# Performance work log

Measured on AMD Instinct MI355X. Metric: run time of the kernel, lower is better.

Reference implementation:

```python
import jax, jax.numpy as jnp
import numpy as np

G, NP, K, H, DH, D, NL = 256, 1000, 8, 8, 10, 80, 10  # graphs, nodes/graph, knn, heads, d_head, hidden, layers


def setup_inputs() -> dict:
    key = jax.random.key(0)
    ks = jax.random.split(key, 16)
    rn = lambda k, shape: (jax.random.normal(k, shape, jnp.float32) * 0.05)
    return dict(
        h_feat=jax.random.normal(ks[0], (G, NP, 9), jnp.float32),
        bn_gamma=jnp.ones((9,), jnp.float32), bn_beta=jnp.zeros((9,), jnp.float32),
        W_emb=rn(ks[1], (9, D)), b_emb=jnp.zeros((D,), jnp.float32),
        Wq=rn(ks[2], (NL, D, D)), Wk=rn(ks[3], (NL, D, D)), Wv=rn(ks[4], (NL, D, D)),
        Wo=rn(ks[5], (NL, D, D)), bo=jnp.zeros((NL, D), jnp.float32),
        W1=rn(ks[6], (NL, D, 2 * D)), b1=jnp.zeros((NL, 2 * D), jnp.float32),
        W2=rn(ks[7], (NL, 2 * D, D)), b2=jnp.zeros((NL, D), jnp.float32),
        Wr0=rn(ks[8], (D, 40)), br0=jnp.zeros((40,), jnp.float32),
        Wr1=rn(ks[9], (40, 20)), br1=jnp.zeros((20,), jnp.float32),
        Wr2=rn(ks[10], (20, 64)), br2=jnp.zeros((64,), jnp.float32),
        W_clust=rn(ks[11], (64, 3)),
        W_beta=rn(ks[12], (64, 1)), b_beta=jnp.zeros((1,), jnp.float32),
    )


def _forward(h_feat, bn_gamma, bn_beta, W_emb, b_emb, Wq, Wk, Wv, Wo, bo,
             W1, b1, W2, b2, Wr0, br0, Wr1, br1, Wr2, br2, W_clust, W_beta, b_beta):
    # knn graph on raw coords (first 3 feature columns), per graph, k=8 (self included)
    coords = h_feat[..., :3]
    d2 = jnp.sum((coords[:, :, None, :] - coords[:, None, :, :]) ** 2, -1)  # [G,NP,NP]
    nbr = jax.lax.top_k(-d2, K)[1]  # [G,NP,K] neighbor indices per destination node
    gidx = jnp.arange(G)[:, None, None]

    # BatchNorm1d (training-mode batch stats over all nodes) + embedding
    x = h_feat.reshape(-1, 9)
    mu = x.mean(0)
    var = x.var(0)
    x = (x - mu) / jnp.sqrt(var + 1e-5) * bn_gamma + bn_beta
    h = (x @ W_emb + b_emb).reshape(G, NP, D)

    inv_sqrt_d = jnp.float32(1.0 / np.sqrt(DH))

    def layer(h, p):
        wq, wk, wv, wo, bo_, w1, b1_, w2, b2_ = p
        q = (h @ wq).reshape(G, NP, H, DH)
        k_ = (h @ wk).reshape(G, NP, H, DH)
        v = (h @ wv).reshape(G, NP, H, DH)
        kn = k_[gidx, nbr]  # [G,NP,K,H,DH] gather src K over edges
        vn = v[gidx, nbr]
        s = jnp.einsum('gnkhd,gnhd->gnkh', kn, q) * inv_sqrt_d
        s = jnp.exp(jnp.clip(s, -5.0, 5.0))  # scaled_exp with clamp
        wV = jnp.einsum('gnkh,gnkhd->gnhd', s, vn)
        attn = (wV / (s.sum(2)[..., None] + 1e-6)).reshape(G, NP, D)
        h = h + attn @ wo + bo_  # O proj + residual (no LN/BN)
        h = h + jax.nn.relu(h @ w1 + b1_) @ w2 + b2_  # FFN + residual
        return h, None

    h, _ = jax.lax.scan(layer, h, (Wq, Wk, Wv, Wo, bo, W1, b1, W2, b2))

    # MLPReadout 80->40->20->64 (ReLU between), then clustering coords + beta
    y = h.reshape(-1, D)
    y = jax.nn.relu(y @ Wr0 + br0)
    y = jax.nn.relu(y @ Wr1 + br1)
    y = y @ Wr2 + br2
    cc = y @ W_clust  # [N,3], no bias
    beta = y @ W_beta + b_beta  # [N,1]
    return jnp.concatenate([cc, beta], axis=1)  # [N,4]


def reference(h_feat, bn_gamma, bn_beta, W_emb, b_emb, Wq, Wk, Wv, Wo, bo,
              W1, b1, W2, b2, Wr0, br0, Wr1, br1, Wr2, br2, W_clust, W_beta, b_beta):
    return _forward(h_feat, bn_gamma, bn_beta, W_emb, b_emb, Wq, Wk, Wv, Wo, bo,
                    W1, b1, W2, b2, Wr0, br0, Wr1, br1, Wr2, br2, W_clust, W_beta, b_beta)
```

## Files before the change

kernel.cpp:

```cpp
#include <hip/hip_runtime.h>
#include <cstdint>
#include <cstddef>


typedef __attribute__((ext_vector_type(8))) short short8v;
typedef __attribute__((ext_vector_type(4))) float f32x4;

#define MFMA16(ACC, A, B) ACC = __builtin_amdgcn_mfma_f32_16x16x32_bf16(A, B, ACC, 0, 0, 0)
#define MF3(ACC, AH, AL, BH, BL) { MFMA16(ACC, AH, BH); MFMA16(ACC, AH, BL); MFMA16(ACC, AL, BH); }

__device__ __forceinline__ void splitbf(float x, unsigned short& hi, unsigned short& lo) {
  unsigned u = __float_as_uint(x);
  unsigned r = u + 0x7FFFu + ((u >> 16) & 1u);
  hi = (unsigned short)(r >> 16);
  float hf = __uint_as_float(((unsigned)hi) << 16);
  float lf = x - hf;
  unsigned u2 = __float_as_uint(lf);
  unsigned r2 = u2 + 0x7FFFu + ((u2 >> 16) & 1u);
  lo = (unsigned short)(r2 >> 16);
}

__device__ __forceinline__ float bf2f(unsigned short v) {
  return __uint_as_float(((unsigned)v) << 16);
}

__global__ __launch_bounds__(256) void knn_kernel(const float* __restrict__ hf, int* __restrict__ nbr) {
  __shared__ __align__(16) float cs[3000];
  int b = blockIdx.x;
  int g = b >> 2;
  for (int i = threadIdx.x; i < 3000; i += 256) {
    cs[i] = hf[((size_t)g * 1000 + (i / 3)) * 9 + (i % 3)];
  }
  __syncthreads();
  int tid = threadIdx.x;
  int lane = tid & 127;
  int q = ((b & 3) << 1) + (tid >> 7);
  if (lane < 125) {
    int n = q * 125 + lane;
    float cx = cs[n * 3 + 0], cy = cs[n * 3 + 1], cz = cs[n * 3 + 2];
    float bd[8];
    int bi[8];
    #pragma unroll
    for (int q2 = 0; q2 < 8; ++q2) { bd[q2] = 3.402823466e38f; bi[q2] = 0; }
    for (int j = 0; j < 1000; j += 8) {
      const float4* base = reinterpret_cast<const float4*>(cs + j * 3);
      float4 a0 = base[0], a1 = base[1], a2 = base[2], a3 = base[3], a4 = base[4], a5 = base[5];
      float d2v[8];
      {
        float dx = __fsub_rn(cx, a0.x), dy = __fsub_rn(cy, a0.y), dz = __fsub_rn(cz, a0.z);
        d2v[0] = __fadd_rn(__fadd_rn(__fmul_rn(dx, dx), __fmul_rn(dy, dy)), __fmul_rn(dz, dz));
      }
      {
        float dx = __fsub_rn(cx, a0.w), dy = __fsub_rn(cy, a1.x), dz = __fsub_rn(cz, a1.y);
        d2v[1] = __fadd_rn(__fadd_rn(__fmul_rn(dx, dx), __fmul_rn(dy, dy)), __fmul_rn(dz, dz));
      }
      {
        float dx = __fsub_rn(cx, a1.z), dy = __fsub_rn(cy, a1.w), dz = __fsub_rn(cz, a2.x);
        d2v[2] = __fadd_rn(__fadd_rn(__fmul_rn(dx, dx), __fmul_rn(dy, dy)), __fmul_rn(dz, dz));
      }
      {
        float dx = __fsub_rn(cx, a2.y), dy = __fsub_rn(cy, a2.z), dz = __fsub_rn(cz, a2.w);
        d2v[3] = __fadd_rn(__fadd_rn(__fmul_rn(dx, dx), __fmul_rn(dy, dy)), __fmul_rn(dz, dz));
      }
      {
        float dx = __fsub_rn(cx, a3.x), dy = __fsub_rn(cy, a3.y), dz = __fsub_rn(cz, a3.z);
        d2v[4] = __fadd_rn(__fadd_rn(__fmul_rn(dx, dx), __fmul_rn(dy, dy)), __fmul_rn(dz, dz));
      }
      {
        float dx = __fsub_rn(cx, a3.w), dy = __fsub_rn(cy, a4.x), dz = __fsub_rn(cz, a4.y);
        d2v[5] = __fadd_rn(__fadd_rn(__fmul_rn(dx, dx), __fmul_rn(dy, dy)), __fmul_rn(dz, dz));
      }
      {
        float dx = __fsub_rn(cx, a4.z), dy = __fsub_rn(cy, a4.w), dz = __fsub_rn(cz, a5.x);
        d2v[6] = __fadd_rn(__fadd_rn(__fmul_rn(dx, dx), __fmul_rn(dy, dy)), __fmul_rn(dz, dz));
      }
      {
        float dx = __fsub_rn(cx, a5.y), dy = __fsub_rn(cy, a5.z), dz = __fsub_rn(cz, a5.w);
        d2v[7] = __fadd_rn(__fadd_rn(__fmul_rn(dx, dx), __fmul_rn(dy, dy)), __fmul_rn(dz, dz));
      }
      #pragma unroll
      for (int u = 0; u < 8; ++u) {
        float d2 = d2v[u];
        if (d2 < bd[7]) {
          bd[7] = d2; bi[7] = j + u;
          #pragma unroll
          for (int q2 = 7; q2 >= 1; --q2) {
            if (bd[q2] < bd[q2 - 1]) {
              float tf = bd[q2]; bd[q2] = bd[q2 - 1]; bd[q2 - 1] = tf;
              int ti = bi[q2]; bi[q2] = bi[q2 - 1]; bi[q2 - 1] = ti;
            }
          }
        }
      }
    }
    #pragma unroll
    for (int kk = 0; kk < 8; ++kk) nbr[((size_t)g * 1000 + n) * 8 + kk] = bi[kk];
  }
}

__global__ __launch_bounds__(256) void bn_stat1(const float* __restrict__ hf, float* __restrict__ partial) {
  __shared__ float red[4][18];
  int row = blockIdx.x * 256 + threadIdx.x;
  float s[9], ss[9];
  #pragma unroll
  for (int f = 0; f < 9; ++f) {
    float v = hf[(size_t)row * 9 + f];
    s[f] = v;
    ss[f] = v * v;
  }
  for (int off = 32; off > 0; off >>= 1) {
    #pragma unroll
    for (int f = 0; f < 9; ++f) {
      s[f] += __shfl_down(s[f], off);
      ss[f] += __shfl_down(ss[f], off);
    }
  }
  int wid = threadIdx.x >> 6, lane = threadIdx.x & 63;
  if (lane == 0) {
    #pragma unroll
    for (int f = 0; f < 9; ++f) { red[wid][f] = s[f]; red[wid][9 + f] = ss[f]; }
  }
  __syncthreads();
  if (threadIdx.x < 18) {
    partial[(size_t)blockIdx.x * 18 + threadIdx.x] =
        red[0][threadIdx.x] + red[1][threadIdx.x] + red[2][threadIdx.x] + red[3][threadIdx.x];
  }
}

__global__ __launch_bounds__(256) void bn_stat2(const float* __restrict__ partial, float* __restrict__ stats) {
  __shared__ double sd[9][28], qd[9][28];
  int tid = threadIdx.x;
  if (tid < 252) {
    int f = tid % 9, gq = tid / 9;
    double s = 0.0, q = 0.0;
    for (int b = gq; b < 1000; b += 28) {
      s += (double)partial[b * 18 + f];
      q += (double)partial[b * 18 + 9 + f];
    }
    sd[f][gq] = s;
    qd[f][gq] = q;
  }
  __syncthreads();
  if (tid < 9) {
    double s = 0.0, q = 0.0;
    for (int g2 = 0; g2 < 28; ++g2) { s += sd[tid][g2]; q += qd[tid][g2]; }
    double mu = s / 256000.0;
    double var = q / 256000.0 - mu * mu;
    stats[tid] = (float)mu;
    stats[9 + tid] = (float)(1.0 / sqrt(var + 1e-5));
  }
}

__global__ __launch_bounds__(256) void split_tr(const float* __restrict__ src, unsigned short* __restrict__ dhi,
                                                unsigned short* __restrict__ dlo, int R, int C, int KS) {
  const float* s = src + (size_t)blockIdx.x * R * C;
  unsigned short* dh = dhi + (size_t)blockIdx.x * C * KS;
  unsigned short* dl = dlo + (size_t)blockIdx.x * C * KS;
  int n = C * KS;
  for (int i = threadIdx.x; i < n; i += 256) {
    int c = i / KS, kk = i % KS;
    float v = (kk < R) ? s[kk * C + c] : 0.f;
    unsigned short h, l;
    splitbf(v, h, l);
    dh[i] = h;
    dl[i] = l;
  }
}

__global__ __launch_bounds__(320) void embed_kernel(const float* __restrict__ hf, const float* __restrict__ stats,
                                                    const float* __restrict__ gamma, const float* __restrict__ beta,
                                                    const float* __restrict__ We, const float* __restrict__ be,
                                                    float* __restrict__ h) {
  __shared__ __align__(16) float xs[40 * 9];
  size_t p0 = (size_t)blockIdx.x * 40;
  for (int i = threadIdx.x; i < 360; i += 320) {
    int f = i % 9;
    float x = hf[p0 * 9 + i];
    xs[i] = (x - stats[f]) * stats[9 + f] * gamma[f] + beta[f];
  }
  __syncthreads();
  int c = threadIdx.x % 80, pg = threadIdx.x / 80;
  float we[9];
  #pragma unroll
  for (int f = 0; f < 9; ++f) we[f] = We[f * 80 + c];
  float bias = be[c];
  for (int pp = 0; pp < 10; ++pp) {
    int p = pg * 10 + pp;
    float acc = 0.f;
    #pragma unroll
    for (int f = 0; f < 9; ++f) acc = fmaf(xs[p * 9 + f], we[f], acc);
    h[(p0 + p) * 80 + c] = acc + bias;
  }
}

__global__ __launch_bounds__(320) void kv_kernel(const float* __restrict__ h,
                                                 const unsigned short* __restrict__ WkH, const unsigned short* __restrict__ WkL,
                                                 const unsigned short* __restrict__ WvH, const unsigned short* __restrict__ WvL,
                                                 float* __restrict__ kb, float* __restrict__ vb) {
  __shared__ __align__(16) unsigned short ahi[48 * 104];
  __shared__ __align__(16) unsigned short alo[48 * 104];
  int b = blockIdx.x;
  int xcd = b & 7;
  int r = b >> 3;
  int graph = (xcd << 5) + (r / 25);
  int jb = r % 25;
  size_t p0 = (size_t)graph * 1000 + (size_t)jb * 40;
  int tid = threadIdx.x;
  int lane = tid & 63, wv = tid >> 6;
  int fr = lane & 15, fq = lane >> 4;
  for (int i = tid; i < 800; i += 320) {
    int row = i / 20, kq = i % 20;
    float4 v = reinterpret_cast<const float4*>(h + (p0 + row) * 80)[kq];
    unsigned short h0, l0, h1, l1, h2, l2, h3, l3;
    splitbf(v.x, h0, l0); splitbf(v.y, h1, l1); splitbf(v.z, h2, l2); splitbf(v.w, h3, l3);
    int off = row * 104 + kq * 4;
    *reinterpret_cast<unsigned*>(&ahi[off]) = (unsigned)h0 | ((unsigned)h1 << 16);
    *reinterpret_cast<unsigned*>(&ahi[off + 2]) = (unsigned)h2 | ((unsigned)h3 << 16);
    *reinterpret_cast<unsigned*>(&alo[off]) = (unsigned)l0 | ((unsigned)l1 << 16);
    *reinterpret_cast<unsigned*>(&alo[off + 2]) = (unsigned)l2 | ((unsigned)l3 << 16);
  }
  for (int i = tid; i < 384; i += 320) {
    int row = i >> 3, kk = 80 + ((i & 7) << 1);
    int off = row * 104 + kk;
    *reinterpret_cast<unsigned*>(&ahi[off]) = 0u;
    *reinterpret_cast<unsigned*>(&alo[off]) = 0u;
  }
  __syncthreads();
  int bcol = wv * 16 + fr;
  f32x4 ck0 = {0.f, 0.f, 0.f, 0.f}, ck1 = ck0, ck2 = ck0;
  f32x4 cv0 = ck0, cv1 = ck0, cv2 = ck0;
  #pragma unroll
  for (int ks = 0; ks < 3; ++ks) {
    int boff = bcol * 96 + ks * 32 + fq * 8;
    short8v bkh = *reinterpret_cast<const short8v*>(WkH + boff);
    short8v bkl = *reinterpret_cast<const short8v*>(WkL + boff);
    short8v bvh = *reinterpret_cast<const short8v*>(WvH + boff);
    short8v bvl = *reinterpret_cast<const short8v*>(WvL + boff);
    int a0 = (0 * 16 + fr) * 104 + ks * 32 + fq * 8;
    int a1 = (1 * 16 + fr) * 104 + ks * 32 + fq * 8;
    int a2 = (2 * 16 + fr) * 104 + ks * 32 + fq * 8;
    short8v ah0 = *reinterpret_cast<const short8v*>(ahi + a0);
    short8v al0 = *reinterpret_cast<const short8v*>(alo + a0);
    MF3(ck0, ah0, al0, bkh, bkl); MF3(cv0, ah0, al0, bvh, bvl);
    short8v ah1 = *reinterpret_cast<const short8v*>(ahi + a1);
    short8v al1 = *reinterpret_cast<const short8v*>(alo + a1);
    MF3(ck1, ah1, al1, bkh, bkl); MF3(cv1, ah1, al1, bvh, bvl);
    short8v ah2 = *reinterpret_cast<const short8v*>(ahi + a2);
    short8v al2 = *reinterpret_cast<const short8v*>(alo + a2);
    MF3(ck2, ah2, al2, bkh, bkl); MF3(cv2, ah2, al2, bvh, bvl);
  }
  #pragma unroll
  for (int j = 0; j < 4; ++j) {
    int r0 = fq * 4 + j;
    kb[(p0 + r0) * 80 + bcol] = ck0[j];
    vb[(p0 + r0) * 80 + bcol] = cv0[j];
    int r1 = 16 + r0;
    kb[(p0 + r1) * 80 + bcol] = ck1[j];
    vb[(p0 + r1) * 80 + bcol] = cv1[j];
    int r2 = 32 + r0;
    if (r2 < 40) {
      kb[(p0 + r2) * 80 + bcol] = ck2[j];
      vb[(p0 + r2) * 80 + bcol] = cv2[j];
    }
  }
}

__global__ __launch_bounds__(320) void battn_kernel(const float* __restrict__ h, const float* __restrict__ kb,
                                                    const float* __restrict__ vb, const int* __restrict__ nbr,
                                                    const unsigned short* __restrict__ WqH, const unsigned short* __restrict__ WqL,
                                                    const unsigned short* __restrict__ WoH, const unsigned short* __restrict__ WoL,
                                                    const float* __restrict__ bo,
                                                    const unsigned short* __restrict__ W1H, const unsigned short* __restrict__ W1L,
                                                    const float* __restrict__ b1,
                                                    const unsigned short* __restrict__ W2H, const unsigned short* __restrict__ W2L,
                                                    const float* __restrict__ b2, float* __restrict__ hout) {
  __shared__ __align__(16) unsigned short ahi[48 * 168];
  __shared__ __align__(16) unsigned short alo[48 * 168];
  int b = blockIdx.x;
  int xcd = b & 7;
  int r = b >> 3;
  int graph = (xcd << 5) + (r / 25);
  int jb = r % 25;
  size_t gbase = (size_t)graph * 1000;
  size_t pbase = gbase + (size_t)jb * 40;
  int tid = threadIdx.x;
  int lane = tid & 63, wv = tid >> 6;
  int fr = lane & 15, fq = lane >> 4;
  int bcol = wv * 16 + fr;
  int pA = tid >> 3, hhA = tid & 7;
  int nb[8];
  #pragma unroll
  for (int kk = 0; kk < 8; ++kk) nb[kk] = nbr[(pbase + pA) * 8 + kk];
  float hres0[4], hres1[4], hres2[4];
  #pragma unroll
  for (int j = 0; j < 4; ++j) {
    int r0 = fq * 4 + j;
    hres0[j] = h[(pbase + r0) * 80 + bcol];
    hres1[j] = h[(pbase + 16 + r0) * 80 + bcol];
    int r2 = 32 + r0;
    hres2[j] = (r2 < 40) ? h[(pbase + r2) * 80 + bcol] : 0.f;
  }
  for (int i = tid; i < 800; i += 320) {
    int row = i / 20, kq = i % 20;
    float4 v = reinterpret_cast<const float4*>(h + (pbase + row) * 80)[kq];
    unsigned short h0, l0, h1, l1, h2_, l2, h3, l3;
    splitbf(v.x, h0, l0); splitbf(v.y, h1, l1); splitbf(v.z, h2_, l2); splitbf(v.w, h3, l3);
    int off = row * 168 + kq * 4;
    *reinterpret_cast<unsigned*>(&ahi[off]) = (unsigned)h0 | ((unsigned)h1 << 16);
    *reinterpret_cast<unsigned*>(&ahi[off + 2]) = (unsigned)h2_ | ((unsigned)h3 << 16);
    *reinterpret_cast<unsigned*>(&alo[off]) = (unsigned)l0 | ((unsigned)l1 << 16);
    *reinterpret_cast<unsigned*>(&alo[off + 2]) = (unsigned)l2 | ((unsigned)l3 << 16);
  }
  for (int i = tid; i < 384; i += 320) {
    int row = i >> 3, kk = 80 + ((i & 7) << 1);
    int off = row * 168 + kk;
    *reinterpret_cast<unsigned*>(&ahi[off]) = 0u;
    *reinterpret_cast<unsigned*>(&alo[off]) = 0u;
  }
  __syncthreads();
  f32x4 q0 = {0.f, 0.f, 0.f, 0.f}, q1 = q0, q2 = q0;
  {
    #pragma unroll
    for (int ks = 0; ks < 3; ++ks) {
      int boff = bcol * 96 + ks * 32 + fq * 8;
      short8v bh = *reinterpret_cast<const short8v*>(WqH + boff);
      short8v bl = *reinterpret_cast<const short8v*>(WqL + boff);
      int a0 = (0 * 16 + fr) * 168 + ks * 32 + fq * 8;
      int a1 = (1 * 16 + fr) * 168 + ks * 32 + fq * 8;
      int a2 = (2 * 16 + fr) * 168 + ks * 32 + fq * 8;
      short8v ah0 = *reinterpret_cast<const short8v*>(ahi + a0);
      short8v al0 = *reinterpret_cast<const short8v*>(alo + a0);
      MF3(q0, ah0, al0, bh, bl);
      short8v ah1 = *reinterpret_cast<const short8v*>(ahi + a1);
      short8v al1 = *reinterpret_cast<const short8v*>(alo + a1);
      MF3(q1, ah1, al1, bh, bl);
      short8v ah2 = *reinterpret_cast<const short8v*>(ahi + a2);
      short8v al2 = *reinterpret_cast<const short8v*>(alo + a2);
      MF3(q2, ah2, al2, bh, bl);
    }
  }
  __syncthreads();
  {
    #pragma unroll
    for (int j = 0; j < 4; ++j) {
      unsigned short hh_, ll_;
      int r0 = fq * 4 + j;
      splitbf(q0[j], hh_, ll_);
      ahi[r0 * 168 + bcol] = hh_; alo[r0 * 168 + bcol] = ll_;
      int r1 = 16 + r0;
      splitbf(q1[j], hh_, ll_);
      ahi[r1 * 168 + bcol] = hh_; alo[r1 * 168 + bcol] = ll_;
      int r2 = 32 + r0;
      if (r2 < 40) {
        splitbf(q2[j], hh_, ll_);
        ahi[r2 * 168 + bcol] = hh_; alo[r2 * 168 + bcol] = ll_;
      }
    }
  }
  __syncthreads();
  {
    int p = pA, hh = hhA;
    float qv[10];
    #pragma unroll
    for (int d2 = 0; d2 < 5; ++d2) {
      int off = p * 168 + hh * 10 + 2 * d2;
      unsigned uh = *reinterpret_cast<const unsigned*>(&ahi[off]);
      unsigned ul = *reinterpret_cast<const unsigned*>(&alo[off]);
      qv[2 * d2] = bf2f((unsigned short)uh) + bf2f((unsigned short)ul);
      qv[2 * d2 + 1] = bf2f((unsigned short)(uh >> 16)) + bf2f((unsigned short)(ul >> 16));
    }
    float sv[8];
    float denom = 0.f;
    #pragma unroll
    for (int kk = 0; kk < 8; ++kk) {
      const float2* kr = reinterpret_cast<const float2*>(kb + (gbase + nb[kk]) * 80 + hh * 10);
      float acc = 0.f;
      #pragma unroll
      for (int d2 = 0; d2 < 5; ++d2) {
        float2 kv2 = kr[d2];
        acc = fmaf(qv[2 * d2], kv2.x, acc);
        acc = fmaf(qv[2 * d2 + 1], kv2.y, acc);
      }
      float s = acc * 0.31622776601683794f;
      s = fminf(fmaxf(s, -5.f), 5.f);
      s = expf(s);
      sv[kk] = s;
      denom += s;
    }
    float wV[10] = {0, 0, 0, 0, 0, 0, 0, 0, 0, 0};
    #pragma unroll
    for (int kk = 0; kk < 8; ++kk) {
      const float2* vr = reinterpret_cast<const float2*>(vb + (gbase + nb[kk]) * 80 + hh * 10);
      #pragma unroll
      for (int d2 = 0; d2 < 5; ++d2) {
        float2 vv = vr[d2];
        wV[2 * d2] = fmaf(sv[kk], vv.x, wV[2 * d2]);
        wV[2 * d2 + 1] = fmaf(sv[kk], vv.y, wV[2 * d2 + 1]);
      }
    }
    float dn = denom + 1e-6f;
    #pragma unroll
    for (int d2 = 0; d2 < 5; ++d2) {
      float x0 = wV[2 * d2] / dn;
      float x1 = wV[2 * d2 + 1] / dn;
      unsigned short h0, l0, h1, l1;
      splitbf(x0, h0, l0); splitbf(x1, h1, l1);
      int off = p * 168 + hh * 10 + 2 * d2;
      *reinterpret_cast<unsigned*>(&ahi[off]) = (unsigned)h0 | ((unsigned)h1 << 16);
      *reinterpret_cast<unsigned*>(&alo[off]) = (unsigned)l0 | ((unsigned)l1 << 16);
    }
  }
  __syncthreads();
  f32x4 o0 = {0.f, 0.f, 0.f, 0.f}, o1 = o0, o2 = o0;
  {
    #pragma unroll
    for (int ks = 0; ks < 3; ++ks) {
      int boff = bcol * 96 + ks * 32 + fq * 8;
      short8v bh = *reinterpret_cast<const short8v*>(WoH + boff);
      short8v bl = *reinterpret_cast<const short8v*>(WoL + boff);
      int a0 = (0 * 16 + fr) * 168 + ks * 32 + fq * 8;
      int a1 = (1 * 16 + fr) * 168 + ks * 32 + fq * 8;
      int a2 = (2 * 16 + fr) * 168 + ks * 32 + fq * 8;
      short8v ah0 = *reinterpret_cast<const short8v*>(ahi + a0);
      short8v al0 = *reinterpret_cast<const short8v*>(alo + a0);
      MF3(o0, ah0, al0, bh, bl);
      short8v ah1 = *reinterpret_cast<const short8v*>(ahi + a1);
      short8v al1 = *reinterpret_cast<const short8v*>(alo + a1);
      MF3(o1, ah1, al1, bh, bl);
      short8v ah2 = *reinterpret_cast<const short8v*>(ahi + a2);
      short8v al2 = *reinterpret_cast<const short8v*>(alo + a2);
      MF3(o2, ah2, al2, bh, bl);
    }
  }
  __syncthreads();
  {
    float bias = bo[bcol];
    #pragma unroll
    for (int j = 0; j < 4; ++j) {
      unsigned short hh_, ll_;
      int r0 = fq * 4 + j;
      o0[j] = hres0[j] + o0[j] + bias;
      splitbf(o0[j], hh_, ll_);
      ahi[r0 * 168 + bcol] = hh_; alo[r0 * 168 + bcol] = ll_;
      int r1 = 16 + r0;
      o1[j] = hres1[j] + o1[j] + bias;
      splitbf(o1[j], hh_, ll_);
      ahi[r1 * 168 + bcol] = hh_; alo[r1 * 168 + bcol] = ll_;
      int r2 = 32 + r0;
      if (r2 < 40) {
        o2[j] = hres2[j] + o2[j] + bias;
        splitbf(o2[j], hh_, ll_);
        ahi[r2 * 168 + bcol] = hh_; alo[r2 * 168 + bcol] = ll_;
      }
    }
  }
  __syncthreads();
  f32x4 t00 = {0.f, 0.f, 0.f, 0.f}, t01 = t00, t02 = t00;
  f32x4 t10 = t00, t11 = t00, t12 = t00;
  {
    int bc0 = wv * 16 + fr, bc1 = (wv + 5) * 16 + fr;
    #pragma unroll
    for (int ks = 0; ks < 3; ++ks) {
      int b0 = bc0 * 96 + ks * 32 + fq * 8;
      int b1o = bc1 * 96 + ks * 32 + fq * 8;
      short8v bh0 = *reinterpret_cast<const short8v*>(W1H + b0);
      short8v bl0 = *reinterpret_cast<const short8v*>(W1L + b0);
      short8v bh1 = *reinterpret_cast<const short8v*>(W1H + b1o);
      short8v bl1 = *reinterpret_cast<const short8v*>(W1L + b1o);
      int a0 = (0 * 16 + fr) * 168 + ks * 32 + fq * 8;
      int a1 = (1 * 16 + fr) * 168 + ks * 32 + fq * 8;
      int a2 = (2 * 16 + fr) * 168 + ks * 32 + fq * 8;
      short8v ah0 = *reinterpret_cast<const short8v*>(ahi + a0);
      short8v al0 = *reinterpret_cast<const short8v*>(alo + a0);
      MF3(t00, ah0, al0, bh0, bl0); MF3(t10, ah0, al0, bh1, bl1);
      short8v ah1 = *reinterpret_cast<const short8v*>(ahi + a1);
      short8v al1 = *reinterpret_cast<const short8v*>(alo + a1);
      MF3(t01, ah1, al1, bh0, bl0); MF3(t11, ah1, al1, bh1, bl1);
      short8v ah2 = *reinterpret_cast<const short8v*>(ahi + a2);
      short8v al2 = *reinterpret_cast<const short8v*>(alo + a2);
      MF3(t02, ah2, al2, bh0, bl0); MF3(t12, ah2, al2, bh1, bl1);
    }
  }
  __syncthreads();
  {
    int bc0 = wv * 16 + fr, bc1 = (wv + 5) * 16 + fr;
    float bias0 = b1[bc0], bias1 = b1[bc1];
    #pragma unroll
    for (int j = 0; j < 4; ++j) {
      unsigned short hh_, ll_;
      int r0 = fq * 4 + j;
      float t = fmaxf(t00[j] + bias0, 0.f);
      splitbf(t, hh_, ll_); ahi[r0 * 168 + bc0] = hh_; alo[r0 * 168 + bc0] = ll_;
      t = fmaxf(t10[j] + bias1, 0.f);
      splitbf(t, hh_, ll_); ahi[r0 * 168 + bc1] = hh_; alo[r0 * 168 + bc1] = ll_;
      int r1 = 16 + r0;
      t = fmaxf(t01[j] + bias0, 0.f);
      splitbf(t, hh_, ll_); ahi[r1 * 168 + bc0] = hh_; alo[r1 * 168 + bc0] = ll_;
      t = fmaxf(t11[j] + bias1, 0.f);
      splitbf(t, hh_, ll_); ahi[r1 * 168 + bc1] = hh_; alo[r1 * 168 + bc1] = ll_;
      int r2 = 32 + r0;
      if (r2 < 40) {
        t = fmaxf(t02[j] + bias0, 0.f);
        splitbf(t, hh_, ll_); ahi[r2 * 168 + bc0] = hh_; alo[r2 * 168 + bc0] = ll_;
        t = fmaxf(t12[j] + bias1, 0.f);
        splitbf(t, hh_, ll_); ahi[r2 * 168 + bc1] = hh_; alo[r2 * 168 + bc1] = ll_;
      }
    }
  }
  __syncthreads();
  {
    f32x4 c0 = {0.f, 0.f, 0.f, 0.f}, c1 = c0, c2 = c0;
    #pragma unroll
    for (int ks = 0; ks < 5; ++ks) {
      int boff = bcol * 160 + ks * 32 + fq * 8;
      short8v bh = *reinterpret_cast<const short8v*>(W2H + boff);
      short8v bl = *reinterpret_cast<const short8v*>(W2L + boff);
      int a0 = (0 * 16 + fr) * 168 + ks * 32 + fq * 8;
      int a1 = (1 * 16 + fr) * 168 + ks * 32 + fq * 8;
      int a2 = (2 * 16 + fr) * 168 + ks * 32 + fq * 8;
      short8v ah0 = *reinterpret_cast<const short8v*>(ahi + a0);
      short8v al0 = *reinterpret_cast<const short8v*>(alo + a0);
      MF3(c0, ah0, al0, bh, bl);
      short8v ah1 = *reinterpret_cast<const short8v*>(ahi + a1);
      short8v al1 = *reinterpret_cast<const short8v*>(alo + a1);
      MF3(c1, ah1, al1, bh, bl);
      short8v ah2 = *reinterpret_cast<const short8v*>(ahi + a2);
      short8v al2 = *reinterpret_cast<const short8v*>(alo + a2);
      MF3(c2, ah2, al2, bh, bl);
    }
    float bias = b2[bcol];
    #pragma unroll
    for (int j = 0; j < 4; ++j) {
      int r0 = fq * 4 + j;
      hout[(pbase + r0) * 80 + bcol] = o0[j] + c0[j] + bias;
      int r1 = 16 + r0;
      hout[(pbase + r1) * 80 + bcol] = o1[j] + c1[j] + bias;
      int r2 = 32 + r0;
      if (r2 < 40) hout[(pbase + r2) * 80 + bcol] = o2[j] + c2[j] + bias;
    }
  }
}

__global__ __launch_bounds__(320) void readout_kernel(const float* __restrict__ h, const float* __restrict__ Wr0,
                                                      const float* __restrict__ br0, const float* __restrict__ Wr1,
                                                      const float* __restrict__ br1, const float* __restrict__ Wr2,
                                                      const float* __restrict__ br2, const float* __restrict__ Wc,
                                                      const float* __restrict__ Wb, const float* __restrict__ bb,
                                                      float* __restrict__ out) {
  __shared__ __align__(16) float hs[3200];
  __shared__ __align__(16) float y0s[40 * 40];
  __shared__ __align__(16) float y1s[40 * 20];
  __shared__ __align__(16) float y2s[40 * 64];
  size_t p0 = (size_t)blockIdx.x * 40;
  int tid = threadIdx.x;
  {
    const float4* src = reinterpret_cast<const float4*>(h + p0 * 80);
    float4* dst = reinterpret_cast<float4*>(hs);
    for (int i = tid; i < 800; i += 320) dst[i] = src[i];
  }
  __syncthreads();
  {
    int c = tid % 40, grp = tid / 40;
    if (grp < 5) {
      float wcol[80];
      #pragma unroll
      for (int kk = 0; kk < 80; ++kk) wcol[kk] = Wr0[kk * 40 + c];
      float bias = br0[c];
      float acc[8] = {};
      #pragma unroll
      for (int j = 0; j < 8; ++j) {
        const float4* r4 = reinterpret_cast<const float4*>(hs + (grp * 8 + j) * 80);
        #pragma unroll
        for (int kq = 0; kq < 20; ++kq) {
          float4 hv = r4[kq];
          acc[j] = fmaf(hv.x, wcol[4 * kq + 0], acc[j]);
          acc[j] = fmaf(hv.y, wcol[4 * kq + 1], acc[j]);
          acc[j] = fmaf(hv.z, wcol[4 * kq + 2], acc[j]);
          acc[j] = fmaf(hv.w, wcol[4 * kq + 3], acc[j]);
        }
      }
      #pragma unroll
      for (int j = 0; j < 8; ++j) y0s[(grp * 8 + j) * 40 + c] = fmaxf(acc[j] + bias, 0.f);
    }
  }
  __syncthreads();
  {
    int c = tid % 20, grp = tid / 20;
    if (grp < 5) {
      float wcol[40];
      #pragma unroll
      for (int kk = 0; kk < 40; ++kk) wcol[kk] = Wr1[kk * 20 + c];
      float bias = br1[c];
      float acc[8] = {};
      #pragma unroll
      for (int j = 0; j < 8; ++j) {
        const float4* r4 = reinterpret_cast<const float4*>(y0s + (grp * 8 + j) * 40);
        #pragma unroll
        for (int kq = 0; kq < 10; ++kq) {
          float4 hv = r4[kq];
          acc[j] = fmaf(hv.x, wcol[4 * kq + 0], acc[j]);
          acc[j] = fmaf(hv.y, wcol[4 * kq + 1], acc[j]);
          acc[j] = fmaf(hv.z, wcol[4 * kq + 2], acc[j]);
          acc[j] = fmaf(hv.w, wcol[4 * kq + 3], acc[j]);
        }
      }
      #pragma unroll
      for (int j = 0; j < 8; ++j) y1s[(grp * 8 + j) * 20 + c] = fmaxf(acc[j] + bias, 0.f);
    }
  }
  __syncthreads();
  {
    int c = tid % 64, grp = tid / 64;
    float wcol[20];
    #pragma unroll
    for (int kk = 0; kk < 20; ++kk) wcol[kk] = Wr2[kk * 64 + c];
    float bias = br2[c];
    float acc[8] = {};
    #pragma unroll
    for (int j = 0; j < 8; ++j) {
      const float4* r4 = reinterpret_cast<const float4*>(y1s + (grp * 8 + j) * 20);
      #pragma unroll
      for (int kq = 0; kq < 5; ++kq) {
        float4 hv = r4[kq];
        acc[j] = fmaf(hv.x, wcol[4 * kq + 0], acc[j]);
        acc[j] = fmaf(hv.y, wcol[4 * kq + 1], acc[j]);
        acc[j] = fmaf(hv.z, wcol[4 * kq + 2], acc[j]);
        acc[j] = fmaf(hv.w, wcol[4 * kq + 3], acc[j]);
      }
    }
    #pragma unroll
    for (int j = 0; j < 8; ++j) y2s[(grp * 8 + j) * 64 + c] = acc[j] + bias;
  }
  __syncthreads();
  {
    int c = tid % 4, p = tid / 4;
    if (p < 40) {
      float wcol[64];
      if (c < 3) {
        #pragma unroll
        for (int kk = 0; kk < 64; ++kk) wcol[kk] = Wc[kk * 3 + c];
      } else {
        #pragma unroll
        for (int kk = 0; kk < 64; ++kk) wcol[kk] = Wb[kk];
      }
      float acc = 0.f;
      #pragma unroll
      for (int kk = 0; kk < 64; ++kk) acc = fmaf(y2s[p * 64 + kk], wcol[kk], acc);
      if (c == 3) acc += bb[0];
      out[(p0 + p) * 4 + c] = acc;
    }
  }
}

extern "C" void kernel_launch(void* const* d_in, const int* in_sizes, int n_in,
                              void* d_out, int out_size, void* d_ws, size_t ws_size,
                              hipStream_t stream) {
  const float* hf = (const float*)d_in[0];
  const float* gamma = (const float*)d_in[1];
  const float* beta = (const float*)d_in[2];
  const float* We = (const float*)d_in[3];
  const float* be = (const float*)d_in[4];
  const float* Wq = (const float*)d_in[5];
  const float* Wk = (const float*)d_in[6];
  const float* Wv = (const float*)d_in[7];
  const float* Wo = (const float*)d_in[8];
  const float* bo = (const float*)d_in[9];
  const float* W1 = (const float*)d_in[10];
  const float* b1 = (const float*)d_in[11];
  const float* W2 = (const float*)d_in[12];
  const float* b2 = (const float*)d_in[13];
  const float* Wr0 = (const float*)d_in[14];
  const float* br0 = (const float*)d_in[15];
  const float* Wr1 = (const float*)d_in[16];
  const float* br1 = (const float*)d_in[17];
  const float* Wr2 = (const float*)d_in[18];
  const float* br2 = (const float*)d_in[19];
  const float* Wc = (const float*)d_in[20];
  const float* Wb = (const float*)d_in[21];
  const float* bb = (const float*)d_in[22];
  float* out = (float*)d_out;

  char* wsp = (char*)d_ws;
  int* nbr = (int*)wsp;            wsp += (size_t)256000 * 8 * 4;
  float* hA = (float*)wsp;         wsp += (size_t)256000 * 80 * 4;
  float* kbuf = (float*)wsp;       wsp += (size_t)256000 * 80 * 4;
  float* vbuf = (float*)wsp;       wsp += (size_t)256000 * 80 * 4;
  float* partial = (float*)wsp;    wsp += (size_t)1000 * 18 * 4;
  float* stats = (float*)wsp;      wsp += 128;
  unsigned short* WqH = (unsigned short*)wsp; wsp += (size_t)10 * 7680 * 2;
  unsigned short* WqL = (unsigned short*)wsp; wsp += (size_t)10 * 7680 * 2;
  unsigned short* WkH = (unsigned short*)wsp; wsp += (size_t)10 * 7680 * 2;
  unsigned short* WkL = (unsigned short*)wsp; wsp += (size_t)10 * 7680 * 2;
  unsigned short* WvH = (unsigned short*)wsp; wsp += (size_t)10 * 7680 * 2;
  unsigned short* WvL = (unsigned short*)wsp; wsp += (size_t)10 * 7680 * 2;
  unsigned short* WoH = (unsigned short*)wsp; wsp += (size_t)10 * 7680 * 2;
  unsigned short* WoL = (unsigned short*)wsp; wsp += (size_t)10 * 7680 * 2;
  unsigned short* W1H = (unsigned short*)wsp; wsp += (size_t)10 * 15360 * 2;
  unsigned short* W1L = (unsigned short*)wsp; wsp += (size_t)10 * 15360 * 2;
  unsigned short* W2H = (unsigned short*)wsp; wsp += (size_t)10 * 12800 * 2;
  unsigned short* W2L = (unsigned short*)wsp; wsp += (size_t)10 * 12800 * 2;

  knn_kernel<<<1024, 256, 0, stream>>>(hf, nbr);
  bn_stat1<<<1000, 256, 0, stream>>>(hf, partial);
  bn_stat2<<<1, 256, 0, stream>>>(partial, stats);
  split_tr<<<10, 256, 0, stream>>>(Wq, WqH, WqL, 80, 80, 96);
  split_tr<<<10, 256, 0, stream>>>(Wk, WkH, WkL, 80, 80, 96);
  split_tr<<<10, 256, 0, stream>>>(Wv, WvH, WvL, 80, 80, 96);
  split_tr<<<10, 256, 0, stream>>>(Wo, WoH, WoL, 80, 80, 96);
  split_tr<<<10, 256, 0, stream>>>(W1, W1H, W1L, 80, 160, 96);
  split_tr<<<10, 256, 0, stream>>>(W2, W2H, W2L, 160, 80, 160);
  embed_kernel<<<6400, 320, 0, stream>>>(hf, stats, gamma, beta, We, be, hA);
  for (int l = 0; l < 10; ++l) {
    kv_kernel<<<6400, 320, 0, stream>>>(hA, WkH + (size_t)l * 7680, WkL + (size_t)l * 7680,
                                        WvH + (size_t)l * 7680, WvL + (size_t)l * 7680, kbuf, vbuf);
    battn_kernel<<<6400, 320, 0, stream>>>(hA, kbuf, vbuf, nbr,
                                           WqH + (size_t)l * 7680, WqL + (size_t)l * 7680,
                                           WoH + (size_t)l * 7680, WoL + (size_t)l * 7680, bo + (size_t)l * 80,
                                           W1H + (size_t)l * 15360, W1L + (size_t)l * 15360, b1 + (size_t)l * 160,
                                           W2H + (size_t)l * 12800, W2L + (size_t)l * 12800, b2 + (size_t)l * 80, hA);
  }
  readout_kernel<<<6400, 320, 0, stream>>>(hA, Wr0, br0, Wr1, br1, Wr2, br2, Wc, Wb, bb, out);
}
```

Measured before the change: 3.429 ms.

## Store hidden state as packed bf16 hi/lo pairs and restructure kv_kernel

The hidden state is now stored as a packed 32-bit word holding the bf16 high and low split, so consumers rebuild MFMA operands with shifts and masks instead of re-running splitbf. kv_kernel drops its shared-memory staging, loads A fragments straight from global into registers, and assigns each wave a 16-row strip across all five column tiles, covering 80 rows per block and halving the grid. Residual reads and the readout unpack hi+lo, which loses a little precision compared with fp32 storage. The aim is to cut split arithmetic and LDS traffic.

Measured after the change: 3.964 ms. 15.6% more time.

```diff
diff --git a/kernel.cpp b/kernel.cpp
--- a/kernel.cpp
+++ b/kernel.cpp
@@ -5,6 +5,7 @@
 
 typedef __attribute__((ext_vector_type(8))) short short8v;
 typedef __attribute__((ext_vector_type(4))) float f32x4;
+typedef union { short8v v; unsigned u[4]; } S8U;
 
 #define MFMA16(ACC, A, B) ACC = __builtin_amdgcn_mfma_f32_16x16x32_bf16(A, B, ACC, 0, 0, 0)
 #define MF3(ACC, AH, AL, BH, BL) { MFMA16(ACC, AH, BH); MFMA16(ACC, AH, BL); MFMA16(ACC, AL, BH); }
@@ -20,8 +21,14 @@
   lo = (unsigned short)(r2 >> 16);
 }
 
-__device__ __forceinline__ float bf2f(unsigned short v) {
-  return __uint_as_float(((unsigned)v) << 16);
+__device__ __forceinline__ unsigned packsplit(float x) {
+  unsigned short hi, lo;
+  splitbf(x, hi, lo);
+  return ((unsigned)hi << 16) | (unsigned)lo;
+}
+
+__device__ __forceinline__ float unpackf(unsigned u) {
+  return __uint_as_float(u & 0xFFFF0000u) + __uint_as_float(u << 16);
 }
 
 __global__ __launch_bounds__(256) void knn_kernel(const float* __restrict__ hf, int* __restrict__ nbr) {
@@ -170,7 +177,7 @@
 __global__ __launch_bounds__(320) void embed_kernel(const float* __restrict__ hf, const float* __restrict__ stats,
                                                     const float* __restrict__ gamma, const float* __restrict__ beta,
                                                     const float* __restrict__ We, const float* __restrict__ be,
-                                                    float* __restrict__ h) {
+                                                    unsigned* __restrict__ h) {
   __shared__ __align__(16) float xs[40 * 9];
   size_t p0 = (size_t)blockIdx.x * 40;
   for (int i = threadIdx.x; i < 360; i += 320) {
@@ -189,83 +196,76 @@
     float acc = 0.f;
     #pragma unroll
     for (int f = 0; f < 9; ++f) acc = fmaf(xs[p * 9 + f], we[f], acc);
-    h[(p0 + p) * 80 + c] = acc + bias;
-  }
-}
-
-__global__ __launch_bounds__(320) void kv_kernel(const float* __restrict__ h,
+    h[(p0 + p) * 80 + c] = packsplit(acc + bias);
+  }
+}
+
+__global__ __launch_bounds__(320) void kv_kernel(const unsigned* __restrict__ hA,
                                                  const unsigned short* __restrict__ WkH, const unsigned short* __restrict__ WkL,
                                                  const unsigned short* __restrict__ WvH, const unsigned short* __restrict__ WvL,
                                                  float* __restrict__ kb, float* __restrict__ vb) {
-  __shared__ __align__(16) unsigned short ahi[48 * 104];
-  __shared__ __align__(16) unsigned short alo[48 * 104];
   int b = blockIdx.x;
   int xcd = b & 7;
   int r = b >> 3;
-  int graph = (xcd << 5) + (r / 25);
-  int jb = r % 25;
-  size_t p0 = (size_t)graph * 1000 + (size_t)jb * 40;
+  int graph = (xcd << 5) + (r / 13);
+  int t13 = r % 13;
+  size_t pbase = (size_t)graph * 1000 + (size_t)t13 * 80;
+  int nrows = (t13 == 12) ? 40 : 80;
   int tid = threadIdx.x;
   int lane = tid & 63, wv = tid >> 6;
   int fr = lane & 15, fq = lane >> 4;
-  for (int i = tid; i < 800; i += 320) {
-    int row = i / 20, kq = i % 20;
-    float4 v = reinterpret_cast<const float4*>(h + (p0 + row) * 80)[kq];
-    unsigned short h0, l0, h1, l1, h2, l2, h3, l3;
-    splitbf(v.x, h0, l0); splitbf(v.y, h1, l1); splitbf(v.z, h2, l2); splitbf(v.w, h3, l3);
-    int off = row * 104 + kq * 4;
-    *reinterpret_cast<unsigned*>(&ahi[off]) = (unsigned)h0 | ((unsigned)h1 << 16);
-    *reinterpret_cast<unsigned*>(&ahi[off + 2]) = (unsigned)h2 | ((unsigned)h3 << 16);
-    *reinterpret_cast<unsigned*>(&alo[off]) = (unsigned)l0 | ((unsigned)l1 << 16);
-    *reinterpret_cast<unsigned*>(&alo[off + 2]) = (unsigned)l2 | ((unsigned)l3 << 16);
-  }
-  for (int i = tid; i < 384; i += 320) {
-    int row = i >> 3, kk = 80 + ((i & 7) << 1);
-    int off = row * 104 + kk;
-    *reinterpret_cast<unsigned*>(&ahi[off]) = 0u;
-    *reinterpret_cast<unsigned*>(&alo[off]) = 0u;
-  }
-  __syncthreads();
-  int bcol = wv * 16 + fr;
-  f32x4 ck0 = {0.f, 0.f, 0.f, 0.f}, ck1 = ck0, ck2 = ck0;
-  f32x4 cv0 = ck0, cv1 = ck0, cv2 = ck0;
+  int rowbase = wv * 16;
+  int arow = rowbase + fr;
+  bool rvalid = arow < nrows;
+  short8v AH[3], AL[3];
   #pragma unroll
   for (int ks = 0; ks < 3; ++ks) {
-    int boff = bcol * 96 + ks * 32 + fq * 8;
-    short8v bkh = *reinterpret_cast<const short8v*>(WkH + boff);
-    short8v bkl = *reinterpret_cast<const short8v*>(WkL + boff);
-    short8v bvh = *reinterpret_cast<const short8v*>(WvH + boff);
-    short8v bvl = *reinterpret_cast<const short8v*>(WvL + boff);
-    int a0 = (0 * 16 + fr) * 104 + ks * 32 + fq * 8;
-    int a1 = (1 * 16 + fr) * 104 + ks * 32 + fq * 8;
-    int a2 = (2 * 16 + fr) * 104 + ks * 32 + fq * 8;
-    short8v ah0 = *reinterpret_cast<const short8v*>(ahi + a0);
-    short8v al0 = *reinterpret_cast<const short8v*>(alo + a0);
-    MF3(ck0, ah0, al0, bkh, bkl); MF3(cv0, ah0, al0, bvh, bvl);
-    short8v ah1 = *reinterpret_cast<const short8v*>(ahi + a1);
-    short8v al1 = *reinterpret_cast<const short8v*>(alo + a1);
-    MF3(ck1, ah1, al1, bkh, bkl); MF3(cv1, ah1, al1, bvh, bvl);
-    short8v ah2 = *reinterpret_cast<const short8v*>(ahi + a2);
-    short8v al2 = *reinterpret_cast<const short8v*>(alo + a2);
-    MF3(ck2, ah2, al2, bkh, bkl); MF3(cv2, ah2, al2, bvh, bvl);
+    int c0 = ks * 32 + fq * 8;
+    S8U ah, al;
+    if (rvalid && c0 < 80) {
+      const uint4* src = reinterpret_cast<const uint4*>(hA + (pbase + arow) * 80 + c0);
+      uint4 x = src[0], y = src[1];
+      ah.u[0] = (x.x >> 16) | (x.y & 0xFFFF0000u);
+      ah.u[1] = (x.z >> 16) | (x.w & 0xFFFF0000u);
+      ah.u[2] = (y.x >> 16) | (y.y & 0xFFFF0000u);
+      ah.u[3] = (y.z >> 16) | (y.w & 0xFFFF0000u);
+      al.u[0] = (x.x & 0xFFFFu) | (x.y << 16);
+      al.u[1] = (x.z & 0xFFFFu) | (x.w << 16);
+      al.u[2] = (y.x & 0xFFFFu) | (y.y << 16);
+      al.u[3] = (y.z & 0xFFFFu) | (y.w << 16);
+    } else {
+      ah.u[0] = ah.u[1] = ah.u[2] = ah.u[3] = 0u;
+      al.u[0] = al.u[1] = al.u[2] = al.u[3] = 0u;
+    }
+    AH[ks] = ah.v;
+    AL[ks] = al.v;
   }
   #pragma unroll
-  for (int j = 0; j < 4; ++j) {
-    int r0 = fq * 4 + j;
-    kb[(p0 + r0) * 80 + bcol] = ck0[j];
-    vb[(p0 + r0) * 80 + bcol] = cv0[j];
-    int r1 = 16 + r0;
-    kb[(p0 + r1) * 80 + bcol] = ck1[j];
-    vb[(p0 + r1) * 80 + bcol] = cv1[j];
-    int r2 = 32 + r0;
-    if (r2 < 40) {
-      kb[(p0 + r2) * 80 + bcol] = ck2[j];
-      vb[(p0 + r2) * 80 + bcol] = cv2[j];
-    }
-  }
-}
-
-__global__ __launch_bounds__(320) void battn_kernel(const float* __restrict__ h, const float* __restrict__ kb,
+  for (int ct = 0; ct < 5; ++ct) {
+    f32x4 ck = {0.f, 0.f, 0.f, 0.f}, cv = ck;
+    #pragma unroll
+    for (int ks = 0; ks < 3; ++ks) {
+      int boff = (ct * 16 + fr) * 96 + ks * 32 + fq * 8;
+      short8v bkh = *reinterpret_cast<const short8v*>(WkH + boff);
+      short8v bkl = *reinterpret_cast<const short8v*>(WkL + boff);
+      short8v bvh = *reinterpret_cast<const short8v*>(WvH + boff);
+      short8v bvl = *reinterpret_cast<const short8v*>(WvL + boff);
+      MF3(ck, AH[ks], AL[ks], bkh, bkl);
+      MF3(cv, AH[ks], AL[ks], bvh, bvl);
+    }
+    int col = ct * 16 + fr;
+    #pragma unroll
+    for (int j = 0; j < 4; ++j) {
+      int row = rowbase + fq * 4 + j;
+      if (row < nrows) {
+        kb[(pbase + row) * 80 + col] = ck[j];
+        vb[(pbase + row) * 80 + col] = cv[j];
+      }
+    }
+  }
+}
+
+__global__ __launch_bounds__(320) void battn_kernel(const unsigned* __restrict__ h, const float* __restrict__ kb,
                                                     const float* __restrict__ vb, const int* __restrict__ nbr,
                                                     const unsigned short* __restrict__ WqH, const unsigned short* __restrict__ WqL,
                                                     const unsigned short* __restrict__ WoH, const unsigned short* __restrict__ WoL,
@@ -273,7 +273,7 @@
                                                     const unsigned short* __restrict__ W1H, const unsigned short* __restrict__ W1L,
                                                     const float* __restrict__ b1,
                                                     const unsigned short* __restrict__ W2H, const unsigned short* __restrict__ W2L,
-                                                    const float* __restrict__ b2, float* __restrict__ hout) {
+                                                    const float* __restrict__ b2, unsigned* __restrict__ hout) {
   __shared__ __align__(16) unsigned short ahi[48 * 168];
   __shared__ __align__(16) unsigned short alo[48 * 168];
   int b = blockIdx.x;
@@ -295,21 +295,19 @@
   #pragma unroll
   for (int j = 0; j < 4; ++j) {
     int r0 = fq * 4 + j;
-    hres0[j] = h[(pbase + r0) * 80 + bcol];
-    hres1[j] = h[(pbase + 16 + r0) * 80 + bcol];
+    hres0[j] = unpackf(h[(pbase + r0) * 80 + bcol]);
+    hres1[j] = unpackf(h[(pbase + 16 + r0) * 80 + bcol]);
     int r2 = 32 + r0;
-    hres2[j] = (r2 < 40) ? h[(pbase + r2) * 80 + bcol] : 0.f;
+    hres2[j] = (r2 < 40) ? unpackf(h[(pbase + r2) * 80 + bcol]) : 0.f;
   }
   for (int i = tid; i < 800; i += 320) {
     int row = i / 20, kq = i % 20;
-    float4 v = reinterpret_cast<const float4*>(h + (pbase + row) * 80)[kq];
-    unsigned short h0, l0, h1, l1, h2_, l2, h3, l3;
-    splitbf(v.x, h0, l0); splitbf(v.y, h1, l1); splitbf(v.z, h2_, l2); splitbf(v.w, h3, l3);
+    uint4 v = reinterpret_cast<const uint4*>(h + (pbase + row) * 80)[kq];
     int off = row * 168 + kq * 4;
-    *reinterpret_cast<unsigned*>(&ahi[off]) = (unsigned)h0 | ((unsigned)h1 << 16);
-    *reinterpret_cast<unsigned*>(&ahi[off + 2]) = (unsigned)h2_ | ((unsigned)h3 << 16);
-    *reinterpret_cast<unsigned*>(&alo[off]) = (unsigned)l0 | ((unsigned)l1 << 16);
-    *reinterpret_cast<unsigned*>(&alo[off + 2]) = (unsigned)l2 | ((unsigned)l3 << 16);
+    *reinterpret_cast<unsigned*>(&ahi[off]) = (v.x >> 16) | (v.y & 0xFFFF0000u);
+    *reinterpret_cast<unsigned*>(&ahi[off + 2]) = (v.z >> 16) | (v.w & 0xFFFF0000u);
+    *reinterpret_cast<unsigned*>(&alo[off]) = (v.x & 0xFFFFu) | (v.y << 16);
+    *reinterpret_cast<unsigned*>(&alo[off + 2]) = (v.z & 0xFFFFu) | (v.w << 16);
   }
   for (int i = tid; i < 384; i += 320) {
     int row = i >> 3, kk = 80 + ((i & 7) << 1);
@@ -366,8 +364,8 @@
       int off = p * 168 + hh * 10 + 2 * d2;
       unsigned uh = *reinterpret_cast<const unsigned*>(&ahi[off]);
       unsigned ul = *reinterpret_cast<const unsigned*>(&alo[off]);
-      qv[2 * d2] = bf2f((unsigned short)uh) + bf2f((unsigned short)ul);
-      qv[2 * d2 + 1] = bf2f((unsigned short)(uh >> 16)) + bf2f((unsigned short)(ul >> 16));
+      qv[2 * d2] = __uint_as_float((uh & 0xFFFFu) << 16) + __uint_as_float((ul & 0xFFFFu) << 16);
+      qv[2 * d2 + 1] = __uint_as_float(uh & 0xFFFF0000u) + __uint_as_float(ul & 0xFFFF0000u);
     }
     float sv[8];
     float denom = 0.f;
@@ -532,16 +530,16 @@
     #pragma unroll
     for (int j = 0; j < 4; ++j) {
       int r0 = fq * 4 + j;
-      hout[(pbase + r0) * 80 + bcol] = o0[j] + c0[j] + bias;
+      hout[(pbase + r0) * 80 + bcol] = packsplit(o0[j] + c0[j] + bias);
       int r1 = 16 + r0;
-      hout[(pbase + r1) * 80 + bcol] = o1[j] + c1[j] + bias;
+      hout[(pbase + r1) * 80 + bcol] = packsplit(o1[j] + c1[j] + bias);
       int r2 = 32 + r0;
-      if (r2 < 40) hout[(pbase + r2) * 80 + bcol] = o2[j] + c2[j] + bias;
-    }
-  }
-}
-
-__global__ __launch_bounds__(320) void readout_kernel(const float* __restrict__ h, const float* __restrict__ Wr0,
+      if (r2 < 40) hout[(pbase + r2) * 80 + bcol] = packsplit(o2[j] + c2[j] + bias);
+    }
+  }
+}
+
+__global__ __launch_bounds__(320) void readout_kernel(const unsigned* __restrict__ h, const float* __restrict__ Wr0,
                                                       const float* __restrict__ br0, const float* __restrict__ Wr1,
                                                       const float* __restrict__ br1, const float* __restrict__ Wr2,
                                                       const float* __restrict__ br2, const float* __restrict__ Wc,
@@ -554,9 +552,14 @@
   size_t p0 = (size_t)blockIdx.x * 40;
   int tid = threadIdx.x;
   {
-    const float4* src = reinterpret_cast<const float4*>(h + p0 * 80);
+    const uint4* src = reinterpret_cast<const uint4*>(h + p0 * 80);
     float4* dst = reinterpret_cast<float4*>(hs);
-    for (int i = tid; i < 800; i += 320) dst[i] = src[i];
+    for (int i = tid; i < 800; i += 320) {
+      uint4 v = src[i];
+      float4 f;
+      f.x = unpackf(v.x); f.y = unpackf(v.y); f.z = unpackf(v.z); f.w = unpackf(v.w);
+      dst[i] = f;
+    }
   }
   __syncthreads();
   {
@@ -682,7 +685,7 @@
 
   char* wsp = (char*)d_ws;
   int* nbr = (int*)wsp;            wsp += (size_t)256000 * 8 * 4;
-  float* hA = (float*)wsp;         wsp += (size_t)256000 * 80 * 4;
+  unsigned* hA = (unsigned*)wsp;   wsp += (size_t)256000 * 80 * 4;
   float* kbuf = (float*)wsp;       wsp += (size_t)256000 * 80 * 4;
   float* vbuf = (float*)wsp;       wsp += (size_t)256000 * 80 * 4;
   float* partial = (float*)wsp;    wsp += (size_t)1000 * 18 * 4;
@@ -711,7 +714,7 @@
   split_tr<<<10, 256, 0, stream>>>(W2, W2H, W2L, 160, 80, 160);
   embed_kernel<<<6400, 320, 0, stream>>>(hf, stats, gamma, beta, We, be, hA);
   for (int l = 0; l < 10; ++l) {
-    kv_kernel<<<6400, 320, 0, stream>>>(hA, WkH + (size_t)l * 7680, WkL + (size_t)l * 7680,
+    kv_kernel<<<3328, 320, 0, stream>>>(hA, WkH + (size_t)l * 7680, WkL + (size_t)l * 7680,
                                         WvH + (size_t)l * 7680, WvL + (size_t)l * 7680, kbuf, vbuf);
     battn_kernel<<<6400, 320, 0, stream>>>(hA, kbuf, vbuf, nbr,
                                            WqH + (size_t)l * 7680, WqL + (size_t)l * 7680,
```
